# Kernel optimization log

Measured on AMD Instinct MI355X. Metric: run time of the kernel, lower is better.

## Reference

```python
import jax, jax.numpy as jnp
import numpy as np

B, P, H, NO, NA = 8, 16, 32, 32, 8
D, L, NH, F = 768, 12, 12, 3072
DH = D // NH
N = P + H * (NO + NA)  # 1296
NEG = -1e9


def _rule_mask():
    # group ids: 0=task(prefix), 1=obs, 2=action; prefix timestep = -1
    g = np.concatenate([np.zeros(P, np.int32),
                        np.tile(np.concatenate([np.full(NO, 1, np.int32), np.full(NA, 2, np.int32)]), H)])
    t = np.concatenate([np.full(P, -1, np.int32), np.repeat(np.arange(H, dtype=np.int32), NO + NA)])
    ti, tj = t[:, None], t[None, :]
    # attention_rules: everyone attends ALL to task; obs/action attend CAUSAL to obs;
    # action attends CAUSAL to action; task attends ALL to task; all else NEVER.
    rules = {(0, 0): 'all', (1, 0): 'all', (2, 0): 'all',
             (1, 1): 'causal', (2, 1): 'causal', (2, 2): 'causal'}
    m = np.zeros((N, N), bool)
    for (gi, gj), r in rules.items():
        sel = (g[:, None] == gi) & (g[None, :] == gj)
        cond = np.ones((N, N), bool) if r == 'all' else (tj <= ti)
        m |= sel & cond
    return m

RULE_MASK = jnp.asarray(_rule_mask())
SCALE = np.float32(1.0 / np.sqrt(DH))


def _ln(x, s, b):
    mu = x.mean(-1, keepdims=True)
    var = ((x - mu) ** 2).mean(-1, keepdims=True)
    return (x - mu) * jax.lax.rsqrt(var + 1e-6) * s + b


def _forward(prefix_tokens, obs_tokens, act_tokens, ln1_s, ln1_b, ln2_s, ln2_b,
             wq, wk, wv, wo, bq, bk, bv, bo, w1, b1, w2, b2, lnf_s, lnf_b,
             prefix_mask, obs_mask, act_mask):
    # assemble_input_tokens: concat timestep groups on token dim, fold horizon, prepend prefix
    ts = jnp.concatenate([obs_tokens, act_tokens], axis=2).reshape(B, H * (NO + NA), D)
    x = jnp.concatenate([prefix_tokens, ts], axis=1)  # (B, N, D)
    pad = jnp.concatenate(
        [prefix_mask, jnp.concatenate([obs_mask, act_mask], axis=2).reshape(B, -1)], axis=1)
    mask = RULE_MASK[None, None] & pad[:, None, None, :]  # (B,1,N,N), broadcast over heads
    for i in range(L):
        h = _ln(x, ln1_s[i], ln1_b[i])
        q = (h @ wq[i] + bq[i]).reshape(B, N, NH, DH)
        k = (h @ wk[i] + bk[i]).reshape(B, N, NH, DH)
        v = (h @ wv[i] + bv[i]).reshape(B, N, NH, DH)
        s = jnp.einsum('bqhd,bkhd->bhqk', q, k) * SCALE
        a = jax.nn.softmax(jnp.where(mask, s, NEG), axis=-1)
        o = jnp.einsum('bhqk,bkhd->bqhd', a, v).reshape(B, N, D)
        x = x + o @ wo[i] + bo[i]
        h2 = _ln(x, ln2_s[i], ln2_b[i])
        x = x + jax.nn.gelu(h2 @ w1[i] + b1[i]) @ w2[i] + b2[i]
    return _ln(x, lnf_s, lnf_b)


def setup_inputs() -> dict:
    key = jax.random.key(0)
    ks = jax.random.split(key, 9)
    sc = 0.02
    return dict(
        prefix_tokens=jax.random.normal(ks[0], (B, P, D), jnp.float32),
        obs_tokens=jax.random.normal(ks[1], (B, H, NO, D), jnp.float32),
        act_tokens=jax.random.normal(ks[2], (B, H, NA, D), jnp.float32),
        ln1_s=jnp.ones((L, D), jnp.float32), ln1_b=jnp.zeros((L, D), jnp.float32),
        ln2_s=jnp.ones((L, D), jnp.float32), ln2_b=jnp.zeros((L, D), jnp.float32),
        wq=jax.random.normal(ks[3], (L, D, D), jnp.float32) * sc,
        wk=jax.random.normal(ks[4], (L, D, D), jnp.float32) * sc,
        wv=jax.random.normal(ks[5], (L, D, D), jnp.float32) * sc,
        wo=jax.random.normal(ks[6], (L, D, D), jnp.float32) * sc,
        bq=jnp.zeros((L, D), jnp.float32), bk=jnp.zeros((L, D), jnp.float32),
        bv=jnp.zeros((L, D), jnp.float32), bo=jnp.zeros((L, D), jnp.float32),
        w1=jax.random.normal(ks[7], (L, D, F), jnp.float32) * sc,
        b1=jnp.zeros((L, F), jnp.float32),
        w2=jax.random.normal(ks[8], (L, F, D), jnp.float32) * sc,
        b2=jnp.zeros((L, D), jnp.float32),
        lnf_s=jnp.ones((D,), jnp.float32), lnf_b=jnp.zeros((D,), jnp.float32),
        prefix_mask=jnp.ones((B, P), bool),
        obs_mask=jnp.ones((B, H, NO), bool),
        act_mask=jnp.ones((B, H, NA), bool),
    )


def reference(prefix_tokens, obs_tokens, act_tokens, ln1_s, ln1_b, ln2_s, ln2_b,
              wq, wk, wv, wo, bq, bk, bv, bo, w1, b1, w2, b2, lnf_s, lnf_b,
              prefix_mask, obs_mask, act_mask):
    return _forward(prefix_tokens, obs_tokens, act_tokens, ln1_s, ln1_b, ln2_s, ln2_b,
                    wq, wk, wv, wo, bq, bk, bv, bo, w1, b1, w2, b2, lnf_s, lnf_b,
                    prefix_mask, obs_mask, act_mask)
```

## Files before the change

kernel.cpp:

```cpp
#include <hip/hip_runtime.h>

typedef unsigned short u16;
typedef __attribute__((ext_vector_type(8))) __bf16 bf16x8;
typedef __attribute__((ext_vector_type(4))) float floatx4;

#define NTOK 1296
#define BN_TOT 10368
#define DMODEL 768
#define DFF 3072
#define NHEAD 12
#define DHEAD 64
#define NLAYER 12
#define NQT 21
#define SCALE_QK 0.125f

__device__ __forceinline__ u16 f2bf(float f) {
    unsigned u = __builtin_bit_cast(unsigned, f);
    unsigned r = (u + 0x7FFFu + ((u >> 16) & 1u)) >> 16;
    return (u16)r;
}

__device__ __forceinline__ unsigned cvt_pk_bf16(float lo, float hi) {
    unsigned r;
    asm("v_cvt_pk_bf16_f32 %0, %1, %2" : "=v"(r) : "v"(lo), "v"(hi));
    return r;
}

__device__ __forceinline__ float gelu_f(float x) {
    float u = 0.7978845608028654f * (x + 0.044715f * x * x * x);
    float t = 1.f - 2.f / (__expf(2.f * u) + 1.f);
    return 0.5f * x * (1.f + t);
}

__global__ void assemble_x(const float* __restrict__ prefix,
                           const float* __restrict__ obs,
                           const float* __restrict__ act,
                           float* __restrict__ X) {
    int idx = blockIdx.x * 256 + threadIdx.x;
    if (idx >= BN_TOT * DMODEL) return;
    int d = idx % DMODEL;
    int n = (idx / DMODEL) % NTOK;
    int b = idx / (DMODEL * NTOK);
    float v;
    if (n < 16) {
        v = prefix[((size_t)b * 16 + n) * DMODEL + d];
    } else {
        int q = n - 16;
        int m = q / 40, r = q % 40;
        if (r < 32) v = obs[(((size_t)b * 32 + m) * 32 + r) * DMODEL + d];
        else        v = act[(((size_t)b * 32 + m) * 8 + (r - 32)) * DMODEL + d];
    }
    X[idx] = v;
}

__global__ void build_pad(const int* __restrict__ pm,
                          const int* __restrict__ om,
                          const int* __restrict__ am,
                          unsigned char* __restrict__ pad) {
    int idx = blockIdx.x * 256 + threadIdx.x;
    if (idx >= BN_TOT) return;
    int n = idx % NTOK, b = idx / NTOK;
    int v;
    if (n < 16) v = pm[b * 16 + n];
    else {
        int q = n - 16;
        int m = q / 40, r = q % 40;
        v = (r < 32) ? om[(b * 32 + m) * 32 + r] : am[(b * 32 + m) * 8 + (r - 32)];
    }
    pad[idx] = (v != 0) ? 1 : 0;
}

__global__ void build_biascat(const float* __restrict__ bq,
                              const float* __restrict__ bk,
                              const float* __restrict__ bv,
                              float* __restrict__ bc) {
    int idx = blockIdx.x * 256 + threadIdx.x;
    if (idx >= NLAYER * 2304) return;
    int l = idx / 2304, c = idx % 2304;
    int which = c / 768, cc = c % 768;
    const float* src = (which == 0) ? bq : (which == 1) ? bk : bv;
    bc[idx] = src[l * 768 + cc];
}

__global__ void transpose_cvt(const float* __restrict__ src, u16* __restrict__ dst,
                              int K, int Nc, long layerStride) {
    src += (size_t)blockIdx.z * K * Nc;
    dst += (size_t)blockIdx.z * layerStride;
    __shared__ float tile[32][33];
    int n0 = blockIdx.x * 32, k0 = blockIdx.y * 32;
    int tx = threadIdx.x, ty = threadIdx.y;
#pragma unroll
    for (int i = 0; i < 4; ++i)
        tile[ty + i * 8][tx] = src[(size_t)(k0 + ty + i * 8) * Nc + n0 + tx];
    __syncthreads();
#pragma unroll
    for (int i = 0; i < 4; ++i) {
        int n = n0 + ty + i * 8;
        dst[(size_t)n * K + k0 + tx] = f2bf(tile[tx][ty + i * 8]);
    }
}

__global__ __launch_bounds__(256) void ln_kernel(const float* __restrict__ x,
                                                 const float* __restrict__ s,
                                                 const float* __restrict__ bb,
                                                 u16* __restrict__ obf,
                                                 float* __restrict__ of32) {
    int row = blockIdx.x * 4 + (threadIdx.x >> 6);
    int lane = threadIdx.x & 63;
    const float4* xv = (const float4*)(x + (size_t)row * DMODEL);
    float4 v[3];
    v[0] = xv[lane]; v[1] = xv[lane + 64]; v[2] = xv[lane + 128];
    float sum = 0.f, sq = 0.f;
#pragma unroll
    for (int i = 0; i < 3; ++i) {
        sum += v[i].x + v[i].y + v[i].z + v[i].w;
        sq  += v[i].x * v[i].x + v[i].y * v[i].y + v[i].z * v[i].z + v[i].w * v[i].w;
    }
#pragma unroll
    for (int d = 32; d > 0; d >>= 1) {
        sum += __shfl_xor(sum, d);
        sq  += __shfl_xor(sq, d);
    }
    float mu = sum * (1.f / DMODEL);
    float var = sq * (1.f / DMODEL) - mu * mu;
    float rstd = rsqrtf(var + 1e-6f);
    const float4* sv = (const float4*)s;
    const float4* bv = (const float4*)bb;
#pragma unroll
    for (int i = 0; i < 3; ++i) {
        float4 sc = sv[lane + i * 64], bc = bv[lane + i * 64];
        float y0 = (v[i].x - mu) * rstd * sc.x + bc.x;
        float y1 = (v[i].y - mu) * rstd * sc.y + bc.y;
        float y2 = (v[i].z - mu) * rstd * sc.z + bc.z;
        float y3 = (v[i].w - mu) * rstd * sc.w + bc.w;
        size_t base = (size_t)row * DMODEL + i * 256 + lane * 4;
        if (obf) {
            uint2 pk;
            pk.x = (unsigned)f2bf(y0) | ((unsigned)f2bf(y1) << 16);
            pk.y = (unsigned)f2bf(y2) | ((unsigned)f2bf(y3) << 16);
            *(uint2*)&obf[base] = pk;
        } else {
            float4 o = {y0, y1, y2, y3};
            *(float4*)&of32[base] = o;
        }
    }
}

template <int EPI>
__global__ __launch_bounds__(256) void gemm_k(const u16* __restrict__ A,
                                              const u16* __restrict__ Bt,
                                              const float* __restrict__ bias,
                                              const float* __restrict__ resid,
                                              void* __restrict__ outp,
                                              int M, int Nc, int K) {
    __shared__ __attribute__((aligned(16))) u16 As[4096];
    __shared__ __attribute__((aligned(16))) u16 Bs[4096];
    int tid = threadIdx.x;
    int bc = blockIdx.x, br = blockIdx.y;
    int lane = tid & 63, w = tid >> 6;
    int wr = (w >> 1) * 64, wc = (w & 1) * 64;
    int lr = lane & 15, C = lane >> 4;
    floatx4 acc[4][4] = {};

    int r0 = tid >> 2;
    int cph = tid & 3;
    const u16* Abase = A + (size_t)(br * 128) * K;
    const u16* Bbase = Bt + (size_t)(bc * 128) * K;

    for (int k0 = 0; k0 < K; k0 += 32) {
        __syncthreads();
#pragma unroll
        for (int i = 0; i < 2; ++i) {
            int r = i * 64 + r0;
            int cl = cph ^ ((r >> 1) & 3);
            const u16* ga = Abase + (size_t)r * K + k0 + cl * 8;
            const u16* gb = Bbase + (size_t)r * K + k0 + cl * 8;
            __builtin_amdgcn_global_load_lds(
                (const __attribute__((address_space(1))) void*)ga,
                (__attribute__((address_space(3))) void*)&As[(i * 256 + w * 64) * 8], 16, 0, 0);
            __builtin_amdgcn_global_load_lds(
                (const __attribute__((address_space(1))) void*)gb,
                (__attribute__((address_space(3))) void*)&Bs[(i * 256 + w * 64) * 8], 16, 0, 0);
        }
        __syncthreads();
        bf16x8 af[4], bf[4];
#pragma unroll
        for (int i = 0; i < 4; ++i) {
            int R = wr + i * 16 + lr;
            af[i] = *(const bf16x8*)&As[(R * 4 + (C ^ ((R >> 1) & 3))) * 8];
        }
#pragma unroll
        for (int i = 0; i < 4; ++i) {
            int R = wc + i * 16 + lr;
            bf[i] = *(const bf16x8*)&Bs[(R * 4 + (C ^ ((R >> 1) & 3))) * 8];
        }
#pragma unroll
        for (int i = 0; i < 4; ++i)
#pragma unroll
            for (int j = 0; j < 4; ++j)
                acc[i][j] = __builtin_amdgcn_mfma_f32_16x16x32_bf16(af[i], bf[j], acc[i][j], 0, 0, 0);
    }

    int gr0 = br * 128 + wr, gc0 = bc * 128 + wc;
#pragma unroll
    for (int i = 0; i < 4; ++i) {
#pragma unroll
        for (int j = 0; j < 4; ++j) {
#pragma unroll
            for (int r = 0; r < 4; ++r) {
                int grow = gr0 + i * 16 + (lane >> 4) * 4 + r;
                int gcol = gc0 + j * 16 + lr;
                float v = acc[i][j][r] + bias[gcol];
                if constexpr (EPI == 2) {
                    ((u16*)outp)[(size_t)grow * Nc + gcol] = f2bf(gelu_f(v));
                } else if constexpr (EPI == 3) {
                    size_t idx = (size_t)grow * Nc + gcol;
                    ((float*)outp)[idx] = resid[idx] + v;
                } else {
                    int b = grow / NTOK, n = grow % NTOK;
                    int which = gcol / 768;
                    int c = gcol - which * 768;
                    int nh = c >> 6, dh = c & 63;
                    u16* base = (u16*)outp + (size_t)which * ((size_t)BN_TOT * DMODEL);
                    if (which < 2)
                        base[(((size_t)b * NHEAD + nh) * NTOK + n) * DHEAD + dh] = f2bf(v);
                    else
                        base[(((size_t)b * NHEAD + nh) * DHEAD + dh) * NTOK + n] = f2bf(v);
                }
            }
        }
    }
}

__global__ __launch_bounds__(256) void attn_k(const u16* __restrict__ Q,
                                              const u16* __restrict__ Kb,
                                              const u16* __restrict__ Vt,
                                              const unsigned char* __restrict__ pad,
                                              u16* __restrict__ O) {
    __shared__ __attribute__((aligned(16))) u16 Ks[2][64 * 64];
    __shared__ __attribute__((aligned(16))) u16 Vs[2][64 * 64];
    __shared__ __attribute__((aligned(16))) u16 plds[4][16 * 64];

    int wgid = blockIdx.x;
    int xcd = wgid & 7, slot = wgid >> 3;
    int qt = NQT - 1 - (slot % NQT);
    int g = (slot / NQT) * 8 + xcd;
    int b = g / NHEAD, h = g % NHEAD;

    int tid = threadIdx.x, lane = tid & 63, w = tid >> 6;
    int rg = lane >> 4, lc = lane & 15;
    int q0 = qt * 64 + w * 16;
    size_t bh = (size_t)(b * NHEAD + h);

    int lastrow = min(qt * 64 + 63, NTOK - 1);
    int jend = (lastrow < 16) ? 16 : 16 + 40 * ((lastrow - 16) / 40 + 1);
    jend = min(jend, NTOK);
    int njt = (jend + 63) >> 6;

    int q = q0 + lc;
    bool qok = q < NTOK;
    int tmax_obs = -1, tmax_act = -1;
    if (qok && q >= 16) {
        int qi = q - 16;
        int ti = qi / 40;
        bool gact = (qi % 40) >= 32;
        tmax_obs = ti;
        tmax_act = gact ? ti : -1;
    }

    const u16* qb = Q + (bh * NTOK + min(q, NTOK - 1)) * DHEAD;
    bf16x8 qf0, qf1;
    {
        bf16x8 t0 = *(const bf16x8*)(qb + rg * 8);
        bf16x8 t1 = *(const bf16x8*)(qb + 32 + rg * 8);
#pragma unroll
        for (int i = 0; i < 8; ++i) {
            qf0[i] = (__bf16)((float)t0[i] * SCALE_QK);
            qf1[i] = (__bf16)((float)t1[i] * SCALE_QK);
        }
    }

    auto stage = [&](int buf, int jt) {
#pragma unroll
        for (int i = 0; i < 2; ++i) {
            int r = i * 32 + (tid >> 3);
            int cl = (tid & 7) ^ (r & 7);
            const u16* gk = Kb + (bh * NTOK + min(jt * 64 + r, NTOK - 1)) * DHEAD + cl * 8;
            const u16* gv = Vt + (bh * DHEAD + r) * NTOK + jt * 64 + cl * 8;
            __builtin_amdgcn_global_load_lds(
                (const __attribute__((address_space(1))) void*)gk,
                (__attribute__((address_space(3))) void*)&Ks[buf][(i * 256 + w * 64) * 8], 16, 0, 0);
            __builtin_amdgcn_global_load_lds(
                (const __attribute__((address_space(1))) void*)gv,
                (__attribute__((address_space(3))) void*)&Vs[buf][(i * 256 + w * 64) * 8], 16, 0, 0);
        }
    };

    floatx4 oacc[4] = {};
    float mi = -3.0e38f, li = 0.f;
    const unsigned char* padb = pad + (size_t)b * NTOK;

    stage(0, 0);
    __syncthreads();
    int cur = 0;

    for (int jt = 0; jt < njt; ++jt) {
        int j0 = jt * 64;
        if (jt + 1 < njt) stage(cur ^ 1, jt + 1);

        floatx4 s[4];
        __builtin_amdgcn_s_setprio(1);
#pragma unroll
        for (int ct = 0; ct < 4; ++ct) {
            int kk = ct * 16 + lc;
            bf16x8 kf0 = *(const bf16x8*)&Ks[cur][kk * 64 + ((rg ^ (lc & 7)) << 3)];
            bf16x8 kf1 = *(const bf16x8*)&Ks[cur][kk * 64 + (((4 + rg) ^ (lc & 7)) << 3)];
            floatx4 sa = {};
            sa = __builtin_amdgcn_mfma_f32_16x16x32_bf16(kf0, qf0, sa, 0, 0, 0);
            sa = __builtin_amdgcn_mfma_f32_16x16x32_bf16(kf1, qf1, sa, 0, 0, 0);
            s[ct] = sa;
        }
        __builtin_amdgcn_s_setprio(0);

#pragma unroll
        for (int ct = 0; ct < 4; ++ct) {
            int kb0 = j0 + ct * 16 + rg * 4;
            unsigned pw = (kb0 < NTOK) ? *(const unsigned*)(padb + kb0) : 0u;
            bool jpre = kb0 < 16;
            int tj0 = 0, rem0 = 0;
            if (!jpre) { int qj = kb0 - 16; tj0 = qj / 40; rem0 = qj - 40 * tj0; }
#pragma unroll
            for (int r = 0; r < 4; ++r) {
                int key = kb0 + r;
                bool colok = qok && (key < jend) && (((pw >> (8 * r)) & 0xFFu) != 0);
                bool ok;
                if (jpre) ok = colok;
                else {
                    int rem = rem0 + r;
                    int tj = tj0 + (rem >= 40 ? 1 : 0);
                    int remr = rem >= 40 ? rem - 40 : rem;
                    int tm = (remr >= 32) ? tmax_act : tmax_obs;
                    ok = colok && (tj <= tm);
                }
                s[ct][r] = ok ? s[ct][r] : -1.0e9f;
            }
        }
        float mt = fmaxf(fmaxf(fmaxf(s[0][0], s[0][1]), fmaxf(s[0][2], s[0][3])),
                         fmaxf(fmaxf(s[1][0], s[1][1]), fmaxf(s[1][2], s[1][3])));
        float mt2 = fmaxf(fmaxf(fmaxf(s[2][0], s[2][1]), fmaxf(s[2][2], s[2][3])),
                          fmaxf(fmaxf(s[3][0], s[3][1]), fmaxf(s[3][2], s[3][3])));
        mt = fmaxf(mt, mt2);
        mt = fmaxf(mt, __shfl_xor(mt, 16));
        mt = fmaxf(mt, __shfl_xor(mt, 32));
        float mnew = fmaxf(mi, mt);
        float alpha = __expf(mi - mnew);
        float rs = 0.f;
#pragma unroll
        for (int ct = 0; ct < 4; ++ct)
#pragma unroll
            for (int r = 0; r < 4; ++r) {
                float p = __expf(s[ct][r] - mnew);
                s[ct][r] = p;
                rs += p;
            }
        rs += __shfl_xor(rs, 16);
        rs += __shfl_xor(rs, 32);
        li = li * alpha + rs;
        mi = mnew;
#pragma unroll
        for (int ct = 0; ct < 4; ++ct)
#pragma unroll
            for (int r = 0; r < 4; ++r) oacc[ct][r] *= alpha;

#pragma unroll
        for (int ct = 0; ct < 4; ++ct) {
            uint2 pk;
            pk.x = cvt_pk_bf16(s[ct][0], s[ct][1]);
            pk.y = cvt_pk_bf16(s[ct][2], s[ct][3]);
            int chunk = 2 * ct + (rg >> 1);
            int idx = lc * 64 + ((chunk ^ (lc & 7)) << 3) + ((rg & 1) << 2);
            *(uint2*)&plds[w][idx] = pk;
        }
        __builtin_amdgcn_s_setprio(1);
#pragma unroll
        for (int kh = 0; kh < 2; ++kh) {
            bf16x8 pf = *(const bf16x8*)&plds[w][lc * 64 + (((4 * kh + rg) ^ (lc & 7)) << 3)];
#pragma unroll
            for (int ct = 0; ct < 4; ++ct) {
                int dd = ct * 16 + lc;
                bf16x8 vf = *(const bf16x8*)&Vs[cur][dd * 64 + (((kh * 4 + rg) ^ (lc & 7)) << 3)];
                oacc[ct] = __builtin_amdgcn_mfma_f32_16x16x32_bf16(vf, pf, oacc[ct], 0, 0, 0);
            }
        }
        __builtin_amdgcn_s_setprio(0);

        __syncthreads();
        cur ^= 1;
    }

    if (q < NTOK) {
        float inv = 1.f / li;
#pragma unroll
        for (int ct = 0; ct < 4; ++ct) {
            uint2 pk;
            pk.x = cvt_pk_bf16(oacc[ct][0] * inv, oacc[ct][1] * inv);
            pk.y = cvt_pk_bf16(oacc[ct][2] * inv, oacc[ct][3] * inv);
            *(uint2*)&O[((size_t)b * NTOK + q) * DMODEL + h * DHEAD + ct * 16 + rg * 4] = pk;
        }
    }
}

extern "C" void kernel_launch(void* const* d_in, const int* in_sizes, int n_in,
                              void* d_out, int out_size, void* d_ws, size_t ws_size,
                              hipStream_t stream) {
    const float* prefix = (const float*)d_in[0];
    const float* obs    = (const float*)d_in[1];
    const float* act    = (const float*)d_in[2];
    const float* ln1_s  = (const float*)d_in[3];
    const float* ln1_b  = (const float*)d_in[4];
    const float* ln2_s  = (const float*)d_in[5];
    const float* ln2_b  = (const float*)d_in[6];
    const float* wq = (const float*)d_in[7];
    const float* wk = (const float*)d_in[8];
    const float* wv = (const float*)d_in[9];
    const float* wo = (const float*)d_in[10];
    const float* bq = (const float*)d_in[11];
    const float* bk = (const float*)d_in[12];
    const float* bv = (const float*)d_in[13];
    const float* bo = (const float*)d_in[14];
    const float* w1 = (const float*)d_in[15];
    const float* b1 = (const float*)d_in[16];
    const float* w2 = (const float*)d_in[17];
    const float* b2 = (const float*)d_in[18];
    const float* lnf_s = (const float*)d_in[19];
    const float* lnf_b = (const float*)d_in[20];
    const int* pm = (const int*)d_in[21];
    const int* om = (const int*)d_in[22];
    const int* am = (const int*)d_in[23];
    float* out = (float*)d_out;

    char* ws = (char*)d_ws;
    size_t off = 0;
    auto carve = [&](size_t bytes) -> char* {
        char* p = ws + off;
        off += (bytes + 255) & ~(size_t)255;
        return p;
    };
    float* X   = (float*)carve((size_t)BN_TOT * DMODEL * 4);
    u16*   Hb  = (u16*)carve((size_t)BN_TOT * DMODEL * 2);
    u16*   QKV = (u16*)carve((size_t)3 * BN_TOT * DMODEL * 2);
    u16*   Qb  = QKV;
    u16*   Kbf = QKV + (size_t)BN_TOT * DMODEL;
    u16*   Vt  = QKV + (size_t)2 * BN_TOT * DMODEL;
    u16*   Ob  = (u16*)carve((size_t)BN_TOT * DMODEL * 2);
    u16*   MID = (u16*)carve((size_t)BN_TOT * DFF * 2);
    unsigned char* PAD = (unsigned char*)carve(BN_TOT);
    float* BIASC = (float*)carve((size_t)NLAYER * 2304 * 4);
    u16*   WT  = (u16*)carve((size_t)NLAYER * 7077888 * 2);
    if (off > ws_size) return;

    const long LSTR = 7077888;
    const long OWQ = 0, OWO = 1769472, OW1 = 2359296, OW2 = 4718592;
    const long OWK = 589824, OWV = 1179648;

    dim3 blk(256);
    assemble_x<<<(BN_TOT * DMODEL + 255) / 256, blk, 0, stream>>>(prefix, obs, act, X);
    build_pad<<<(BN_TOT + 255) / 256, blk, 0, stream>>>(pm, om, am, PAD);
    build_biascat<<<(NLAYER * 2304 + 255) / 256, blk, 0, stream>>>(bq, bk, bv, BIASC);

    dim3 tb(32, 8);
    transpose_cvt<<<dim3(DMODEL / 32, DMODEL / 32, NLAYER), tb, 0, stream>>>(wq, WT + OWQ, DMODEL, DMODEL, LSTR);
    transpose_cvt<<<dim3(DMODEL / 32, DMODEL / 32, NLAYER), tb, 0, stream>>>(wk, WT + OWK, DMODEL, DMODEL, LSTR);
    transpose_cvt<<<dim3(DMODEL / 32, DMODEL / 32, NLAYER), tb, 0, stream>>>(wv, WT + OWV, DMODEL, DMODEL, LSTR);
    transpose_cvt<<<dim3(DMODEL / 32, DMODEL / 32, NLAYER), tb, 0, stream>>>(wo, WT + OWO, DMODEL, DMODEL, LSTR);
    transpose_cvt<<<dim3(DFF / 32, DMODEL / 32, NLAYER), tb, 0, stream>>>(w1, WT + OW1, DMODEL, DFF, LSTR);
    transpose_cvt<<<dim3(DMODEL / 32, DFF / 32, NLAYER), tb, 0, stream>>>(w2, WT + OW2, DFF, DMODEL, LSTR);

    dim3 g6(DMODEL / 128, BN_TOT / 128);
    dim3 gqkv(2304 / 128, BN_TOT / 128);
    dim3 g24(DFF / 128, BN_TOT / 128);
    dim3 ga(NQT * NHEAD * 8);
    dim3 gln(BN_TOT / 4);

    for (int l = 0; l < NLAYER; ++l) {
        const u16* WTl = WT + (size_t)l * LSTR;
        ln_kernel<<<gln, blk, 0, stream>>>(X, ln1_s + l * DMODEL, ln1_b + l * DMODEL, Hb, nullptr);
        gemm_k<4><<<gqkv, blk, 0, stream>>>(Hb, WTl + OWQ, BIASC + l * 2304, nullptr, Qb, BN_TOT, 2304, DMODEL);
        attn_k<<<ga, blk, 0, stream>>>(Qb, Kbf, Vt, PAD, Ob);
        gemm_k<3><<<g6, blk, 0, stream>>>(Ob, WTl + OWO, bo + l * DMODEL, X, X, BN_TOT, DMODEL, DMODEL);
        ln_kernel<<<gln, blk, 0, stream>>>(X, ln2_s + l * DMODEL, ln2_b + l * DMODEL, Hb, nullptr);
        gemm_k<2><<<g24, blk, 0, stream>>>(Hb, WTl + OW1, b1 + l * DFF, nullptr, MID, BN_TOT, DFF, DMODEL);
        gemm_k<3><<<g6, blk, 0, stream>>>(MID, WTl + OW2, b2 + l * DMODEL, X, X, BN_TOT, DMODEL, DFF);
    }
    ln_kernel<<<gln, blk, 0, stream>>>(X, lnf_s, lnf_b, nullptr, out);
}
```

Before: 5.353 ms.

## Double-buffer GEMM LDS tiles and move attention to 32x32 MFMA with 128-row Q tiles

The GEMM kernel now double-buffers its A/B LDS tiles, prefetching the next K slice while the current one feeds the MFMAs, with one barrier per iteration and raised wave priority around the MFMA block. The attention kernel switches from 16x16x32 to 32x32x16 MFMAs, each wave owning 32 query rows, so a block covers 128 queries and there are about half as many blocks. This is meant to hide global-load latency in the GEMMs and reuse each staged K/V tile across more queries. The costs are double the GEMM LDS footprint and higher register pressure from the larger accumulators, which may lower occupancy.

```diff
diff --git a/kernel.cpp b/kernel.cpp
--- a/kernel.cpp
+++ b/kernel.cpp
@@ -3,6 +3,7 @@
 typedef unsigned short u16;
 typedef __attribute__((ext_vector_type(8))) __bf16 bf16x8;
 typedef __attribute__((ext_vector_type(4))) float floatx4;
+typedef __attribute__((ext_vector_type(16))) float floatx16;
 
 #define NTOK 1296
 #define BN_TOT 10368
@@ -11,7 +12,7 @@
 #define NHEAD 12
 #define DHEAD 64
 #define NLAYER 12
-#define NQT 21
+#define NQT2 11
 #define SCALE_QK 0.125f
 
 __device__ __forceinline__ u16 f2bf(float f) {
@@ -153,8 +154,8 @@
                                               const float* __restrict__ resid,
                                               void* __restrict__ outp,
                                               int M, int Nc, int K) {
-    __shared__ __attribute__((aligned(16))) u16 As[4096];
-    __shared__ __attribute__((aligned(16))) u16 Bs[4096];
+    __shared__ __attribute__((aligned(16))) u16 As[2][4096];
+    __shared__ __attribute__((aligned(16))) u16 Bs[2][4096];
     int tid = threadIdx.x;
     int bc = blockIdx.x, br = blockIdx.y;
     int lane = tid & 63, w = tid >> 6;
@@ -167,8 +168,7 @@
     const u16* Abase = A + (size_t)(br * 128) * K;
     const u16* Bbase = Bt + (size_t)(bc * 128) * K;
 
-    for (int k0 = 0; k0 < K; k0 += 32) {
-        __syncthreads();
+    auto stageg = [&](int buf, int k0) {
 #pragma unroll
         for (int i = 0; i < 2; ++i) {
             int r = i * 64 + r0;
@@ -177,28 +177,39 @@
             const u16* gb = Bbase + (size_t)r * K + k0 + cl * 8;
             __builtin_amdgcn_global_load_lds(
                 (const __attribute__((address_space(1))) void*)ga,
-                (__attribute__((address_space(3))) void*)&As[(i * 256 + w * 64) * 8], 16, 0, 0);
+                (__attribute__((address_space(3))) void*)&As[buf][(i * 256 + w * 64) * 8], 16, 0, 0);
             __builtin_amdgcn_global_load_lds(
                 (const __attribute__((address_space(1))) void*)gb,
-                (__attribute__((address_space(3))) void*)&Bs[(i * 256 + w * 64) * 8], 16, 0, 0);
-        }
-        __syncthreads();
+                (__attribute__((address_space(3))) void*)&Bs[buf][(i * 256 + w * 64) * 8], 16, 0, 0);
+        }
+    };
+
+    stageg(0, 0);
+    __syncthreads();
+    int cur = 0;
+
+    for (int k0 = 0; k0 < K; k0 += 32) {
+        if (k0 + 32 < K) stageg(cur ^ 1, k0 + 32);
         bf16x8 af[4], bf[4];
 #pragma unroll
         for (int i = 0; i < 4; ++i) {
             int R = wr + i * 16 + lr;
-            af[i] = *(const bf16x8*)&As[(R * 4 + (C ^ ((R >> 1) & 3))) * 8];
+            af[i] = *(const bf16x8*)&As[cur][(R * 4 + (C ^ ((R >> 1) & 3))) * 8];
         }
 #pragma unroll
         for (int i = 0; i < 4; ++i) {
             int R = wc + i * 16 + lr;
-            bf[i] = *(const bf16x8*)&Bs[(R * 4 + (C ^ ((R >> 1) & 3))) * 8];
-        }
+            bf[i] = *(const bf16x8*)&Bs[cur][(R * 4 + (C ^ ((R >> 1) & 3))) * 8];
+        }
+        __builtin_amdgcn_s_setprio(1);
 #pragma unroll
         for (int i = 0; i < 4; ++i)
 #pragma unroll
             for (int j = 0; j < 4; ++j)
                 acc[i][j] = __builtin_amdgcn_mfma_f32_16x16x32_bf16(af[i], bf[j], acc[i][j], 0, 0, 0);
+        __builtin_amdgcn_s_setprio(0);
+        __syncthreads();
+        cur ^= 1;
     }
 
     int gr0 = br * 128 + wr, gc0 = bc * 128 + wc;
@@ -239,25 +250,25 @@
                                               u16* __restrict__ O) {
     __shared__ __attribute__((aligned(16))) u16 Ks[2][64 * 64];
     __shared__ __attribute__((aligned(16))) u16 Vs[2][64 * 64];
-    __shared__ __attribute__((aligned(16))) u16 plds[4][16 * 64];
+    __shared__ __attribute__((aligned(16))) u16 plds[4][32 * 64];
 
     int wgid = blockIdx.x;
     int xcd = wgid & 7, slot = wgid >> 3;
-    int qt = NQT - 1 - (slot % NQT);
-    int g = (slot / NQT) * 8 + xcd;
+    int qt = NQT2 - 1 - (slot % NQT2);
+    int g = (slot / NQT2) * 8 + xcd;
     int b = g / NHEAD, h = g % NHEAD;
 
     int tid = threadIdx.x, lane = tid & 63, w = tid >> 6;
-    int rg = lane >> 4, lc = lane & 15;
-    int q0 = qt * 64 + w * 16;
+    int ql = lane & 31, half = lane >> 5;
+    int q0 = qt * 128 + w * 32;
     size_t bh = (size_t)(b * NHEAD + h);
 
-    int lastrow = min(qt * 64 + 63, NTOK - 1);
+    int lastrow = min(qt * 128 + 127, NTOK - 1);
     int jend = (lastrow < 16) ? 16 : 16 + 40 * ((lastrow - 16) / 40 + 1);
     jend = min(jend, NTOK);
     int njt = (jend + 63) >> 6;
 
-    int q = q0 + lc;
+    int q = q0 + ql;
     bool qok = q < NTOK;
     int tmax_obs = -1, tmax_act = -1;
     if (qok && q >= 16) {
@@ -268,15 +279,14 @@
         tmax_act = gact ? ti : -1;
     }
 
-    const u16* qb = Q + (bh * NTOK + min(q, NTOK - 1)) * DHEAD;
-    bf16x8 qf0, qf1;
+    bf16x8 qf[4];
     {
-        bf16x8 t0 = *(const bf16x8*)(qb + rg * 8);
-        bf16x8 t1 = *(const bf16x8*)(qb + 32 + rg * 8);
-#pragma unroll
-        for (int i = 0; i < 8; ++i) {
-            qf0[i] = (__bf16)((float)t0[i] * SCALE_QK);
-            qf1[i] = (__bf16)((float)t1[i] * SCALE_QK);
+        const u16* qb = Q + (bh * NTOK + min(q, NTOK - 1)) * DHEAD + 8 * half;
+#pragma unroll
+        for (int m = 0; m < 4; ++m) {
+            bf16x8 t = *(const bf16x8*)(qb + 16 * m);
+#pragma unroll
+            for (int i = 0; i < 8; ++i) qf[m][i] = (__bf16)((float)t[i] * SCALE_QK);
         }
     }
 
@@ -296,7 +306,7 @@
         }
     };
 
-    floatx4 oacc[4] = {};
+    floatx16 oacc[2] = {};
     float mi = -3.0e38f, li = 0.f;
     const unsigned char* padb = pad + (size_t)b * NTOK;
 
@@ -308,88 +318,93 @@
         int j0 = jt * 64;
         if (jt + 1 < njt) stage(cur ^ 1, jt + 1);
 
-        floatx4 s[4];
+        floatx16 s[2];
         __builtin_amdgcn_s_setprio(1);
 #pragma unroll
-        for (int ct = 0; ct < 4; ++ct) {
-            int kk = ct * 16 + lc;
-            bf16x8 kf0 = *(const bf16x8*)&Ks[cur][kk * 64 + ((rg ^ (lc & 7)) << 3)];
-            bf16x8 kf1 = *(const bf16x8*)&Ks[cur][kk * 64 + (((4 + rg) ^ (lc & 7)) << 3)];
-            floatx4 sa = {};
-            sa = __builtin_amdgcn_mfma_f32_16x16x32_bf16(kf0, qf0, sa, 0, 0, 0);
-            sa = __builtin_amdgcn_mfma_f32_16x16x32_bf16(kf1, qf1, sa, 0, 0, 0);
-            s[ct] = sa;
+        for (int kt = 0; kt < 2; ++kt) {
+            int kk = kt * 32 + ql;
+            floatx16 sa = {};
+#pragma unroll
+            for (int m = 0; m < 4; ++m) {
+                bf16x8 kf = *(const bf16x8*)&Ks[cur][kk * 64 + (((2 * m + half) ^ (kk & 7)) << 3)];
+                sa = __builtin_amdgcn_mfma_f32_32x32x16_bf16(kf, qf[m], sa, 0, 0, 0);
+            }
+            s[kt] = sa;
         }
         __builtin_amdgcn_s_setprio(0);
 
 #pragma unroll
-        for (int ct = 0; ct < 4; ++ct) {
-            int kb0 = j0 + ct * 16 + rg * 4;
-            unsigned pw = (kb0 < NTOK) ? *(const unsigned*)(padb + kb0) : 0u;
-            bool jpre = kb0 < 16;
-            int tj0 = 0, rem0 = 0;
-            if (!jpre) { int qj = kb0 - 16; tj0 = qj / 40; rem0 = qj - 40 * tj0; }
-#pragma unroll
-            for (int r = 0; r < 4; ++r) {
-                int key = kb0 + r;
-                bool colok = qok && (key < jend) && (((pw >> (8 * r)) & 0xFFu) != 0);
-                bool ok;
-                if (jpre) ok = colok;
-                else {
-                    int rem = rem0 + r;
-                    int tj = tj0 + (rem >= 40 ? 1 : 0);
-                    int remr = rem >= 40 ? rem - 40 : rem;
-                    int tm = (remr >= 32) ? tmax_act : tmax_obs;
-                    ok = colok && (tj <= tm);
+        for (int kt = 0; kt < 2; ++kt) {
+#pragma unroll
+            for (int gg = 0; gg < 4; ++gg) {
+                int kb0 = j0 + kt * 32 + 8 * gg + 4 * half;
+                unsigned pw = (kb0 < NTOK) ? *(const unsigned*)(padb + kb0) : 0u;
+                bool jpre = kb0 < 16;
+                int tj0 = 0, rem0 = 0;
+                if (!jpre) { int qj = kb0 - 16; tj0 = qj / 40; rem0 = qj - 40 * tj0; }
+#pragma unroll
+                for (int rr = 0; rr < 4; ++rr) {
+                    int key = kb0 + rr;
+                    bool colok = qok && (key < jend) && (((pw >> (8 * rr)) & 0xFFu) != 0);
+                    bool ok;
+                    if (jpre) ok = colok;
+                    else {
+                        int rem = rem0 + rr;
+                        int tj = tj0 + (rem >= 40 ? 1 : 0);
+                        int remr = rem >= 40 ? rem - 40 : rem;
+                        int tm = (remr >= 32) ? tmax_act : tmax_obs;
+                        ok = colok && (tj <= tm);
+                    }
+                    s[kt][4 * gg + rr] = ok ? s[kt][4 * gg + rr] : -1.0e9f;
                 }
-                s[ct][r] = ok ? s[ct][r] : -1.0e9f;
-            }
-        }
-        float mt = fmaxf(fmaxf(fmaxf(s[0][0], s[0][1]), fmaxf(s[0][2], s[0][3])),
-                         fmaxf(fmaxf(s[1][0], s[1][1]), fmaxf(s[1][2], s[1][3])));
-        float mt2 = fmaxf(fmaxf(fmaxf(s[2][0], s[2][1]), fmaxf(s[2][2], s[2][3])),
-                          fmaxf(fmaxf(s[3][0], s[3][1]), fmaxf(s[3][2], s[3][3])));
-        mt = fmaxf(mt, mt2);
-        mt = fmaxf(mt, __shfl_xor(mt, 16));
+            }
+        }
+
+        float mt = s[0][0];
+#pragma unroll
+        for (int r = 1; r < 16; ++r) mt = fmaxf(mt, s[0][r]);
+#pragma unroll
+        for (int r = 0; r < 16; ++r) mt = fmaxf(mt, s[1][r]);
         mt = fmaxf(mt, __shfl_xor(mt, 32));
         float mnew = fmaxf(mi, mt);
         float alpha = __expf(mi - mnew);
         float rs = 0.f;
 #pragma unroll
-        for (int ct = 0; ct < 4; ++ct)
-#pragma unroll
-            for (int r = 0; r < 4; ++r) {
-                float p = __expf(s[ct][r] - mnew);
-                s[ct][r] = p;
+        for (int kt = 0; kt < 2; ++kt)
+#pragma unroll
+            for (int r = 0; r < 16; ++r) {
+                float p = __expf(s[kt][r] - mnew);
+                s[kt][r] = p;
                 rs += p;
             }
-        rs += __shfl_xor(rs, 16);
         rs += __shfl_xor(rs, 32);
         li = li * alpha + rs;
         mi = mnew;
 #pragma unroll
-        for (int ct = 0; ct < 4; ++ct)
-#pragma unroll
-            for (int r = 0; r < 4; ++r) oacc[ct][r] *= alpha;
-
-#pragma unroll
-        for (int ct = 0; ct < 4; ++ct) {
-            uint2 pk;
-            pk.x = cvt_pk_bf16(s[ct][0], s[ct][1]);
-            pk.y = cvt_pk_bf16(s[ct][2], s[ct][3]);
-            int chunk = 2 * ct + (rg >> 1);
-            int idx = lc * 64 + ((chunk ^ (lc & 7)) << 3) + ((rg & 1) << 2);
-            *(uint2*)&plds[w][idx] = pk;
-        }
+        for (int dt = 0; dt < 2; ++dt)
+#pragma unroll
+            for (int r = 0; r < 16; ++r) oacc[dt][r] *= alpha;
+
+#pragma unroll
+        for (int kt = 0; kt < 2; ++kt)
+#pragma unroll
+            for (int gg = 0; gg < 4; ++gg) {
+                uint2 pk;
+                pk.x = cvt_pk_bf16(s[kt][4 * gg], s[kt][4 * gg + 1]);
+                pk.y = cvt_pk_bf16(s[kt][4 * gg + 2], s[kt][4 * gg + 3]);
+                int c = kt * 4 + gg;
+                *(uint2*)&plds[w][ql * 64 + ((c ^ (ql & 7)) << 3) + 4 * half] = pk;
+            }
+
         __builtin_amdgcn_s_setprio(1);
 #pragma unroll
-        for (int kh = 0; kh < 2; ++kh) {
-            bf16x8 pf = *(const bf16x8*)&plds[w][lc * 64 + (((4 * kh + rg) ^ (lc & 7)) << 3)];
-#pragma unroll
-            for (int ct = 0; ct < 4; ++ct) {
-                int dd = ct * 16 + lc;
-                bf16x8 vf = *(const bf16x8*)&Vs[cur][dd * 64 + (((kh * 4 + rg) ^ (lc & 7)) << 3)];
-                oacc[ct] = __builtin_amdgcn_mfma_f32_16x16x32_bf16(vf, pf, oacc[ct], 0, 0, 0);
+        for (int ks = 0; ks < 4; ++ks) {
+            bf16x8 pf = *(const bf16x8*)&plds[w][ql * 64 + (((2 * ks + half) ^ (ql & 7)) << 3)];
+#pragma unroll
+            for (int dt = 0; dt < 2; ++dt) {
+                int dd = dt * 32 + ql;
+                bf16x8 vf = *(const bf16x8*)&Vs[cur][dd * 64 + (((2 * ks + half) ^ (dd & 7)) << 3)];
+                oacc[dt] = __builtin_amdgcn_mfma_f32_32x32x16_bf16(vf, pf, oacc[dt], 0, 0, 0);
             }
         }
         __builtin_amdgcn_s_setprio(0);
@@ -401,12 +416,15 @@
     if (q < NTOK) {
         float inv = 1.f / li;
 #pragma unroll
-        for (int ct = 0; ct < 4; ++ct) {
-            uint2 pk;
-            pk.x = cvt_pk_bf16(oacc[ct][0] * inv, oacc[ct][1] * inv);
-            pk.y = cvt_pk_bf16(oacc[ct][2] * inv, oacc[ct][3] * inv);
-            *(uint2*)&O[((size_t)b * NTOK + q) * DMODEL + h * DHEAD + ct * 16 + rg * 4] = pk;
-        }
+        for (int dt = 0; dt < 2; ++dt)
+#pragma unroll
+            for (int gg = 0; gg < 4; ++gg) {
+                uint2 pk;
+                pk.x = cvt_pk_bf16(oacc[dt][4 * gg] * inv, oacc[dt][4 * gg + 1] * inv);
+                pk.y = cvt_pk_bf16(oacc[dt][4 * gg + 2] * inv, oacc[dt][4 * gg + 3] * inv);
+                int dbase = dt * 32 + 8 * gg + 4 * half;
+                *(uint2*)&O[((size_t)b * NTOK + q) * DMODEL + h * DHEAD + dbase] = pk;
+            }
     }
 }
 
@@ -479,7 +497,7 @@
     dim3 g6(DMODEL / 128, BN_TOT / 128);
     dim3 gqkv(2304 / 128, BN_TOT / 128);
     dim3 g24(DFF / 128, BN_TOT / 128);
-    dim3 ga(NQT * NHEAD * 8);
+    dim3 ga(NQT2 * NHEAD * 8);
     dim3 gln(BN_TOT / 4);
 
     for (int l = 0; l < NLAYER; ++l) {
```

Result: slower. 5.583 ms (+4.3%).
